# Performance work log

Measured on AMD Instinct MI355X. Metric: run time of the kernel, lower is better.

The kernel has to match this reference:

```python
import jax, jax.numpy as jnp
import numpy as np

T, B, NC, NM, H = 256, 2048, 3, 125, 256  # time, batch, classes, measures, hidden
IN = NC + NM


def setup_inputs() -> dict:
    key = jax.random.key(0)
    ks = jax.random.split(key, 12)
    seq = jax.random.normal(ks[0], (T, B, IN), jnp.float32)
    nan_mask = jax.random.uniform(ks[1], (T, B, IN)) < 0.1
    nan_mask = nan_mask.at[0].set(False)  # first step must be observed
    seq = jnp.where(nan_mask, jnp.nan, seq)
    s = 1.0 / np.sqrt(H)
    u = lambda k, shp: jax.random.uniform(k, shp, jnp.float32, -s, s)
    return {
        "pair_seq": seq,
        "W_ih": u(ks[2], (4 * H, IN)),
        "W_hh": u(ks[3], (4 * H, H)),
        "b_ih": u(ks[4], (4 * H,)),
        "b_hh": u(ks[5], (4 * H,)),
        "W_cat": u(ks[6], (NC, H)),
        "b_cat": u(ks[7], (NC,)),
        "W_val": u(ks[8], (NM, H)),
        "b_val": u(ks[9], (NM,)),
    }


def reference(pair_seq, W_ih, W_hh, b_ih, b_hh, W_cat, b_cat, W_val, b_val):
    cat_seq = pair_seq[:, :, :NC]
    val_seq = pair_seq[:, :, NC:]
    bsz = pair_seq.shape[1]
    h0 = jnp.zeros((bsz, H), pair_seq.dtype)
    c0 = jnp.zeros((bsz, H), pair_seq.dtype)
    # eval mode: dropout masks are all-ones, so they are identity multiplies

    def lstm_cell(x, h, c):
        gates = x @ W_ih.T + b_ih + h @ W_hh.T + b_hh  # [B, 4H]
        i, f, g, o = jnp.split(gates, 4, axis=-1)
        c2 = jax.nn.sigmoid(f) * c + jax.nn.sigmoid(i) * jnp.tanh(g)
        h2 = jax.nn.sigmoid(o) * jnp.tanh(c2)
        return h2, c2

    def step(carry, nxt):
        h, c, i_cat, i_val = carry
        cat_next, val_next = nxt
        x = jnp.concatenate([i_cat, i_val], axis=-1)
        h, c = lstm_cell(x, h, c)
        o_cat = jax.nn.softmax(h @ W_cat.T + b_cat, axis=-1)
        o_val = h @ W_val.T + b_val + i_val
        # impute NaNs in the next timestep with (detached) predictions
        i_cat2 = jnp.where(jnp.isnan(cat_next), jax.lax.stop_gradient(o_cat), cat_next)
        i_val2 = jnp.where(jnp.isnan(val_next), jax.lax.stop_gradient(o_val), val_next)
        return (h, c, i_cat2, i_val2), (o_cat, o_val)

    init = (h0, c0, cat_seq[0], val_seq[0])
    _, (out_cat, out_val) = jax.lax.scan(step, init, (cat_seq[1:], val_seq[1:]))
    return jnp.concatenate([out_cat, out_val], axis=2)  # [T-1, B, NC+NM]
```

## Files before the change

### kernel.cpp

```cpp
#include <hip/hip_runtime.h>
#include <hip/hip_bf16.h>

constexpr int TSTEPS = 255;
constexpr int XROW   = 392;

typedef __attribute__((ext_vector_type(8))) short short8;
typedef __attribute__((ext_vector_type(4))) float f32x4;
typedef __attribute__((ext_vector_type(16))) float f32x16;
typedef __attribute__((ext_vector_type(4))) int i32x4;
typedef __attribute__((ext_vector_type(2))) unsigned int u32x2;

__device__ __forceinline__ unsigned short f2bf(float f) {
    __hip_bfloat16 h = __float2bfloat16(f);
    return *reinterpret_cast<unsigned short*>(&h);
}
__device__ __forceinline__ float bf2f(unsigned short u) {
    __hip_bfloat16 h;
    *reinterpret_cast<unsigned short*>(&h) = u;
    return __bfloat162float(h);
}
__device__ __forceinline__ float sigf(float x) {
    return __builtin_amdgcn_rcpf(1.f + __expf(-x));
}
__device__ __forceinline__ float tanh_fast(float x) {
    x = fminf(fmaxf(x, -15.f), 15.f);
    float e = __expf(-2.f * x);
    return (1.f - e) * __builtin_amdgcn_rcpf(1.f + e);
}

__device__ __forceinline__ i32x4 load_coh16(const void* p) {
    i32x4 r;
    asm volatile("global_load_dwordx4 %0, %1, off sc0 sc1" : "=v"(r) : "v"(p) : "memory");
    return r;
}
__device__ __forceinline__ void store_coh16(void* p, i32x4 v) {
    asm volatile("global_store_dwordx4 %0, %1, off sc0 sc1" :: "v"(p), "v"(v) : "memory");
}

__device__ __forceinline__ void groupbar(unsigned int* cnt, unsigned int tgt, int tid) {
    asm volatile("s_waitcnt vmcnt(0)" ::: "memory");
    __syncthreads();
    if (tid == 0) {
        __hip_atomic_fetch_add(cnt, 1u, __ATOMIC_RELAXED, __HIP_MEMORY_SCOPE_AGENT);
        while (__hip_atomic_load(cnt, __ATOMIC_RELAXED, __HIP_MEMORY_SCOPE_AGENT) < tgt)
            __builtin_amdgcn_s_sleep(1);
    }
    __syncthreads();
}

__global__ void prep_kernel(const float* __restrict__ Wih, const float* __restrict__ Whh,
                            const float* __restrict__ bih, const float* __restrict__ bhh,
                            const float* __restrict__ Wcat, const float* __restrict__ bcat,
                            const float* __restrict__ Wval, const float* __restrict__ bval,
                            unsigned short* __restrict__ Wg, unsigned short* __restrict__ Wo,
                            float* __restrict__ bg, float* __restrict__ bo,
                            unsigned int* __restrict__ flags) {
    int idx = blockIdx.x * 256 + threadIdx.x;
    if (idx < 393216) {
        int j   = idx & 7;
        int l   = (idx >> 3) & 63;
        int t24 = idx >> 9;
        int kt  = t24 % 24;
        int u   = t24 / 24;
        int gm = u & 3, ss = u >> 2;
        int pm = l & 31;
        int n  = (pm & 3) * 256 + ss * 32 + gm * 8 + (pm >> 2);
        int k  = kt * 16 + (l >> 5) * 8 + j;
        float v = (k < 128) ? Wih[n * 128 + k] : Whh[n * 256 + (k - 128)];
        Wg[idx] = f2bf(v);
    } else if (idx < 425984) {
        int i2 = idx - 393216;
        int j = i2 & 7, ll = (i2 >> 3) & 63, kt = (i2 >> 9) & 15, om = i2 >> 13;
        int n = om * 32 + (ll & 31);
        int k = kt * 16 + (ll >> 5) * 8 + j;
        float v = (n < 3) ? Wcat[n * 256 + k] : Wval[(n - 3) * 256 + k];
        Wo[i2] = f2bf(v);
    } else if (idx < 427008) {
        int i3 = idx - 425984;
        bg[i3] = bih[i3] + bhh[i3];
    } else if (idx < 427136) {
        int i4 = idx - 427008;
        bo[i4] = (i4 < 3) ? bcat[i4] : bval[i4 - 3];
    } else if (idx < 428160) {
        flags[idx - 427136] = 0u;
    }
}

__global__ __launch_bounds__(512, 2) void rnn_kernel(
    const float* __restrict__ seq,
    const unsigned short* __restrict__ Wg, const unsigned short* __restrict__ Wo,
    const float* __restrict__ bg, const float* __restrict__ bo,
    unsigned short* __restrict__ hb, unsigned int* __restrict__ flags,
    float* __restrict__ out) {

    __shared__ __align__(16) unsigned short xh[64][XROW];
    __shared__ __align__(16) float bgl[128];
    __shared__ __align__(16) float obl[128];
    extern __shared__ char lds_pad[];
    (void)lds_pad;

    const int tid = threadIdx.x;
    const int wv  = tid >> 6, l = tid & 63;
    const int c   = l & 31, lh = l >> 5;
    const int s   = blockIdx.x >> 5;
    const int r   = blockIdx.x & 31;
    const int row0 = r * 64;
    const int hm  = wv >> 1;
    const int bn  = wv & 1;
    const int R   = bn * 32 + c;
    const bool hm0lh0 = (hm == 0) && (lh == 0);

    unsigned int* cnt = flags + r * 16;

    short8 wga[24], woa[16];
    {
        const short8* WgV = reinterpret_cast<const short8*>(Wg);
        const short8* WoV = reinterpret_cast<const short8*>(Wo);
#pragma unroll
        for (int kt = 0; kt < 24; ++kt) wga[kt] = WgV[(size_t)(((s * 4 + hm) * 24 + kt) * 64) + l];
#pragma unroll
        for (int kt = 0; kt < 16; ++kt) woa[kt] = WoV[(size_t)((hm * 16 + kt) * 64) + l];
    }

    if (tid < 128) {
        int gm_ = tid >> 5, lh_ = (tid >> 4) & 1, i_ = tid & 15;
        int pm = (i_ & 3) + 8 * (i_ >> 2) + 4 * lh_;
        bgl[tid] = bg[(pm & 3) * 256 + s * 32 + gm_ * 8 + (pm >> 2)];
        obl[tid] = bo[gm_ * 32 + 8 * (i_ >> 2) + 4 * lh_ + (i_ & 3)];
    }

#pragma unroll
    for (int i = 0; i < 4; ++i) {
        int ch = i * 512 + tid;
        int row = ch >> 5, c4 = ch & 31;
        f32x4 v = *reinterpret_cast<const f32x4*>(seq + (size_t)(row0 + row) * 128 + c4 * 4);
        unsigned short* p = &xh[row][c4 * 4];
        p[0] = f2bf(v[0]); p[1] = f2bf(v[1]); p[2] = f2bf(v[2]); p[3] = f2bf(v[3]);
    }
    {
        short8 z = {0, 0, 0, 0, 0, 0, 0, 0};
#pragma unroll
        for (int i = 0; i < 4; ++i) {
            int ch = i * 512 + tid;
            int row = ch >> 5, k8 = ch & 31;
            *reinterpret_cast<short8*>(&xh[row][128 + k8 * 8]) = z;
        }
    }

    unsigned int xv[8];
    {
        const float* sp0 = seq + (size_t)(row0 + R) * 128 + hm * 32 + 4 * lh;
#pragma unroll
        for (int g = 0; g < 4; ++g) {
            f32x4 v = *reinterpret_cast<const f32x4*>(sp0 + 8 * g);
            xv[2 * g]     = (unsigned int)f2bf(v[0]) | ((unsigned int)f2bf(v[1]) << 16);
            xv[2 * g + 1] = (unsigned int)f2bf(v[2]) | ((unsigned int)f2bf(v[3]) << 16);
        }
    }

    float cst[4] = {0.f, 0.f, 0.f, 0.f};
    const float* bgp = &bgl[(hm * 2 + lh) * 16];
    const float* obp = &obl[(hm * 2 + lh) * 16];
    const unsigned short* xrow = &xh[R][0];

    __syncthreads();

    for (int t = 0; t < TSTEPS; ++t) {
        f32x4 sq[4];
        if (t < TSTEPS - 1) {
            const float* sp = seq + ((size_t)(t + 1) * 2048 + row0 + R) * 128 + hm * 32 + 4 * lh;
#pragma unroll
            for (int g = 0; g < 4; ++g) sq[g] = *reinterpret_cast<const f32x4*>(sp + 8 * g);
        }

        f32x16 acc, accB;
#pragma unroll
        for (int i = 0; i < 16; ++i) { acc[i] = bgp[i]; accB[i] = 0.f; }
        __builtin_amdgcn_s_setprio(1);
#pragma unroll
        for (int kt = 0; kt < 24; kt += 2) {
            short8 b0 = *reinterpret_cast<const short8*>(xrow + kt * 16 + lh * 8);
            short8 b1 = *reinterpret_cast<const short8*>(xrow + (kt + 1) * 16 + lh * 8);
            acc  = __builtin_amdgcn_mfma_f32_32x32x16_bf16(wga[kt], b0, acc, 0, 0, 0);
            accB = __builtin_amdgcn_mfma_f32_32x32x16_bf16(wga[kt + 1], b1, accB, 0, 0, 0);
        }
        __builtin_amdgcn_s_setprio(0);
#pragma unroll
        for (int i = 0; i < 16; ++i) acc[i] += accB[i];

        float hn[4];
#pragma unroll
        for (int g = 0; g < 4; ++g) {
            float cn = sigf(acc[4 * g + 1]) * cst[g] + sigf(acc[4 * g]) * tanh_fast(acc[4 * g + 2]);
            hn[g] = sigf(acc[4 * g + 3]) * tanh_fast(cn);
            cst[g] = cn;
        }
        {
            i32x4 hw;
#pragma unroll
            for (int g = 0; g < 4; ++g) {
                float other = __shfl_xor(hn[g], 32);
                unsigned short lo = f2bf(lh ? other : hn[g]);
                unsigned short hi = f2bf(lh ? hn[g] : other);
                hw[g] = (int)((unsigned int)lo | ((unsigned int)hi << 16));
            }
            if (lh == 0) {
                char* hp = (char*)hb + (size_t)(t & 1) * 1048576 + (size_t)r * 32768
                         + (size_t)R * 512 + s * 64 + hm * 16;
                store_coh16(hp, hw);
            }
        }

        groupbar(cnt, 8u * (t + 1), tid);

        {
            const unsigned short* hsrc = hb + (size_t)(t & 1) * 524288 + (size_t)r * 16384;
            i32x4 hv[4];
#pragma unroll
            for (int i = 0; i < 4; ++i) {
                int ch = i * 512 + tid;
                hv[i] = load_coh16(hsrc + (size_t)((ch >> 5) * 256 + (ch & 31) * 8));
            }
            asm volatile("s_waitcnt vmcnt(0)" ::: "memory");
            __builtin_amdgcn_sched_barrier(0);
#pragma unroll
            for (int i = 0; i < 4; ++i) {
                int ch = i * 512 + tid;
                *reinterpret_cast<i32x4*>(&xh[ch >> 5][128 + (ch & 31) * 8]) = hv[i];
            }
        }
        __syncthreads();

        f32x16 acc2, acc2B;
#pragma unroll
        for (int i = 0; i < 16; ++i) { acc2[i] = obp[i]; acc2B[i] = 0.f; }
        __builtin_amdgcn_s_setprio(1);
#pragma unroll
        for (int kt = 0; kt < 16; kt += 2) {
            short8 b0 = *reinterpret_cast<const short8*>(xrow + 128 + kt * 16 + lh * 8);
            short8 b1 = *reinterpret_cast<const short8*>(xrow + 128 + (kt + 1) * 16 + lh * 8);
            acc2  = __builtin_amdgcn_mfma_f32_32x32x16_bf16(woa[kt], b0, acc2, 0, 0, 0);
            acc2B = __builtin_amdgcn_mfma_f32_32x32x16_bf16(woa[kt + 1], b1, acc2B, 0, 0, 0);
        }
        __builtin_amdgcn_s_setprio(0);

        float vv[16];
#pragma unroll
        for (int g = 0; g < 4; ++g) {
#pragma unroll
            for (int j = 0; j < 4; ++j) {
                int i = 4 * g + j;
                float v = acc2[i] + acc2B[i];
                unsigned short x16 = (unsigned short)(xv[2 * g + (j >> 1)] >> ((j & 1) * 16));
                bool isCat = (g == 0) && (j < 3) && hm0lh0;
                if (!isCat) v += bf2f(x16);
                vv[i] = v;
            }
        }
        if (hm0lh0) {
            float mx = fmaxf(fmaxf(vv[0], vv[1]), vv[2]);
            float e0 = __expf(vv[0] - mx), e1 = __expf(vv[1] - mx), e2 = __expf(vv[2] - mx);
            float rs = __builtin_amdgcn_rcpf(e0 + e1 + e2);
            vv[0] = e0 * rs; vv[1] = e1 * rs; vv[2] = e2 * rs;
        }

        if (hm == (s >> 1)) {
            int gp = (s & 1) * 2;
            size_t ob0 = ((size_t)t * 2048 + row0 + R) * 128 + hm * 32 + 4 * lh;
            f32x4 o0 = {vv[4 * gp], vv[4 * gp + 1], vv[4 * gp + 2], vv[4 * gp + 3]};
            f32x4 o1 = {vv[4 * gp + 4], vv[4 * gp + 5], vv[4 * gp + 6], vv[4 * gp + 7]};
            *reinterpret_cast<f32x4*>(out + ob0 + 8 * gp) = o0;
            *reinterpret_cast<f32x4*>(out + ob0 + 8 * gp + 8) = o1;
        }
        if (t < TSTEPS - 1) {
#pragma unroll
            for (int g = 0; g < 4; ++g) {
                unsigned int w0 = 0, w1 = 0;
#pragma unroll
                for (int j = 0; j < 4; ++j) {
                    unsigned short s16 = f2bf(sq[g][j]);
                    bool nan = (s16 & 0x7fff) > 0x7f80;
                    unsigned short nv = nan ? f2bf(vv[4 * g + j]) : s16;
                    if (j < 2) w0 |= (unsigned int)nv << (16 * j);
                    else       w1 |= (unsigned int)nv << (16 * (j - 2));
                }
                xv[2 * g] = w0; xv[2 * g + 1] = w1;
                u32x2 wp = {w0, w1};
                *reinterpret_cast<u32x2*>(&xh[R][hm * 32 + 8 * g + 4 * lh]) = wp;
            }
        }
        __syncthreads();
    }
}

extern "C" void kernel_launch(void* const* d_in, const int* in_sizes, int n_in,
                              void* d_out, int out_size, void* d_ws, size_t ws_size,
                              hipStream_t stream) {
    const float* seq  = (const float*)d_in[0];
    const float* Wih  = (const float*)d_in[1];
    const float* Whh  = (const float*)d_in[2];
    const float* bih  = (const float*)d_in[3];
    const float* bhh  = (const float*)d_in[4];
    const float* Wcat = (const float*)d_in[5];
    const float* bcat = (const float*)d_in[6];
    const float* Wval = (const float*)d_in[7];
    const float* bval = (const float*)d_in[8];

    char* ws = (char*)d_ws;
    unsigned short* Wg    = (unsigned short*)(ws);
    unsigned short* Wo    = (unsigned short*)(ws + 786432);
    float*          bgp   = (float*)(ws + 851968);
    float*          bop   = (float*)(ws + 856064);
    unsigned int*   flags = (unsigned int*)(ws + 856576);
    unsigned short* hbuf  = (unsigned short*)(ws + 860672);

    prep_kernel<<<1673, 256, 0, stream>>>(Wih, Whh, bih, bhh, Wcat, bcat, Wval, bval,
                                          Wg, Wo, bgp, bop, flags);
    rnn_kernel<<<256, 512, 32768, stream>>>(seq, Wg, Wo, bgp, bop, hbuf, flags, (float*)d_out);
}
```

Baseline: 1.145 ms.

## Load hidden state directly into MFMA operand registers, skip LDS round-trip

The hidden-state exchange buffer is re-laid out so each lane can global-load its MFMA B-operand fragments directly into registers. The output projection then runs on those registers without the LDS staging and the __syncthreads that preceded it. Only two waves write the loaded h into LDS for the next step's gate GEMM, and these writes are interleaved with the MFMAs. The load is split into two halves with a partial waitcnt so compute can start early. It also drops the dual-accumulator split, packs the next-step inputs to bf16 early, and reads the current inputs back from LDS instead of holding them in registers. This trades more global load traffic per wave and register pressure for fewer barriers on the critical serial path.

Result: slower. 1.697 ms (+48.3%).

```diff
diff --git a/kernel.cpp b/kernel.cpp
--- a/kernel.cpp
+++ b/kernel.cpp
@@ -28,8 +28,8 @@
     return (1.f - e) * __builtin_amdgcn_rcpf(1.f + e);
 }
 
-__device__ __forceinline__ i32x4 load_coh16(const void* p) {
-    i32x4 r;
+__device__ __forceinline__ short8 load_coh16s(const void* p) {
+    short8 r;
     asm volatile("global_load_dwordx4 %0, %1, off sc0 sc1" : "=v"(r) : "v"(p) : "memory");
     return r;
 }
@@ -142,19 +142,7 @@
 #pragma unroll
         for (int i = 0; i < 4; ++i) {
             int ch = i * 512 + tid;
-            int row = ch >> 5, k8 = ch & 31;
-            *reinterpret_cast<short8*>(&xh[row][128 + k8 * 8]) = z;
-        }
-    }
-
-    unsigned int xv[8];
-    {
-        const float* sp0 = seq + (size_t)(row0 + R) * 128 + hm * 32 + 4 * lh;
-#pragma unroll
-        for (int g = 0; g < 4; ++g) {
-            f32x4 v = *reinterpret_cast<const f32x4*>(sp0 + 8 * g);
-            xv[2 * g]     = (unsigned int)f2bf(v[0]) | ((unsigned int)f2bf(v[1]) << 16);
-            xv[2 * g + 1] = (unsigned int)f2bf(v[2]) | ((unsigned int)f2bf(v[3]) << 16);
+            *reinterpret_cast<short8*>(&xh[ch >> 5][128 + (ch & 31) * 8]) = z;
         }
     }
 
@@ -166,11 +154,15 @@
     __syncthreads();
 
     for (int t = 0; t < TSTEPS; ++t) {
-        f32x4 sq[4];
+        unsigned int sqb[8];
         if (t < TSTEPS - 1) {
             const float* sp = seq + ((size_t)(t + 1) * 2048 + row0 + R) * 128 + hm * 32 + 4 * lh;
 #pragma unroll
-            for (int g = 0; g < 4; ++g) sq[g] = *reinterpret_cast<const f32x4*>(sp + 8 * g);
+            for (int g = 0; g < 4; ++g) {
+                f32x4 v = *reinterpret_cast<const f32x4*>(sp + 8 * g);
+                sqb[2 * g]     = (unsigned)f2bf(v[0]) | ((unsigned)f2bf(v[1]) << 16);
+                sqb[2 * g + 1] = (unsigned)f2bf(v[2]) | ((unsigned)f2bf(v[3]) << 16);
+            }
         }
 
         f32x16 acc, accB;
@@ -202,56 +194,62 @@
                 float other = __shfl_xor(hn[g], 32);
                 unsigned short lo = f2bf(lh ? other : hn[g]);
                 unsigned short hi = f2bf(lh ? hn[g] : other);
-                hw[g] = (int)((unsigned int)lo | ((unsigned int)hi << 16));
+                hw[g] = (int)((unsigned)lo | ((unsigned)hi << 16));
             }
             if (lh == 0) {
                 char* hp = (char*)hb + (size_t)(t & 1) * 1048576 + (size_t)r * 32768
-                         + (size_t)R * 512 + s * 64 + hm * 16;
+                         + (size_t)(s * 4 + hm) * 1024 + (size_t)R * 16;
                 store_coh16(hp, hw);
             }
         }
 
         groupbar(cnt, 8u * (t + 1), tid);
 
-        {
-            const unsigned short* hsrc = hb + (size_t)(t & 1) * 524288 + (size_t)r * 16384;
-            i32x4 hv[4];
-#pragma unroll
-            for (int i = 0; i < 4; ++i) {
-                int ch = i * 512 + tid;
-                hv[i] = load_coh16(hsrc + (size_t)((ch >> 5) * 256 + (ch & 31) * 8));
-            }
-            asm volatile("s_waitcnt vmcnt(0)" ::: "memory");
-            __builtin_amdgcn_sched_barrier(0);
-#pragma unroll
-            for (int i = 0; i < 4; ++i) {
-                int ch = i * 512 + tid;
-                *reinterpret_cast<i32x4*>(&xh[ch >> 5][128 + (ch & 31) * 8]) = hv[i];
-            }
-        }
-        __syncthreads();
-
-        f32x16 acc2, acc2B;
-#pragma unroll
-        for (int i = 0; i < 16; ++i) { acc2[i] = obp[i]; acc2B[i] = 0.f; }
+        const char* hbase = (const char*)hb + (size_t)(t & 1) * 1048576
+                          + (size_t)r * 32768 + (size_t)lh * 1024 + (size_t)R * 16;
+        short8 hv0[8], hv1[8];
+        __builtin_amdgcn_sched_barrier(0);
+#pragma unroll
+        for (int q = 0; q < 8; ++q) hv0[q] = load_coh16s(hbase + (size_t)q * 2048);
+#pragma unroll
+        for (int q = 0; q < 8; ++q) hv1[q] = load_coh16s(hbase + (size_t)(8 + q) * 2048);
+        f32x16 acc2;
+#pragma unroll
+        for (int i = 0; i < 16; ++i) acc2[i] = obp[i];
+        asm volatile("s_waitcnt vmcnt(8)" ::: "memory");
+        __builtin_amdgcn_sched_barrier(0);
         __builtin_amdgcn_s_setprio(1);
 #pragma unroll
-        for (int kt = 0; kt < 16; kt += 2) {
-            short8 b0 = *reinterpret_cast<const short8*>(xrow + 128 + kt * 16 + lh * 8);
-            short8 b1 = *reinterpret_cast<const short8*>(xrow + 128 + (kt + 1) * 16 + lh * 8);
-            acc2  = __builtin_amdgcn_mfma_f32_32x32x16_bf16(woa[kt], b0, acc2, 0, 0, 0);
-            acc2B = __builtin_amdgcn_mfma_f32_32x32x16_bf16(woa[kt + 1], b1, acc2B, 0, 0, 0);
-        }
+        for (int kt = 0; kt < 8; ++kt)
+            acc2 = __builtin_amdgcn_mfma_f32_32x32x16_bf16(woa[kt], hv0[kt], acc2, 0, 0, 0);
         __builtin_amdgcn_s_setprio(0);
+        if (wv < 2 && t < TSTEPS - 1) {
+#pragma unroll
+            for (int q = 0; q < 8; ++q)
+                *reinterpret_cast<short8*>(&xh[R][128 + q * 16 + lh * 8]) = hv0[q];
+        }
+        asm volatile("s_waitcnt vmcnt(0)" ::: "memory");
+        __builtin_amdgcn_sched_barrier(0);
+        __builtin_amdgcn_s_setprio(1);
+#pragma unroll
+        for (int kt = 0; kt < 8; ++kt)
+            acc2 = __builtin_amdgcn_mfma_f32_32x32x16_bf16(woa[8 + kt], hv1[kt], acc2, 0, 0, 0);
+        __builtin_amdgcn_s_setprio(0);
+        if (wv < 2 && t < TSTEPS - 1) {
+#pragma unroll
+            for (int q = 0; q < 8; ++q)
+                *reinterpret_cast<short8*>(&xh[R][256 + q * 16 + lh * 8]) = hv1[q];
+        }
 
         float vv[16];
 #pragma unroll
         for (int g = 0; g < 4; ++g) {
+            u32x2 xw = *reinterpret_cast<const u32x2*>(&xh[R][hm * 32 + 8 * g + 4 * lh]);
 #pragma unroll
             for (int j = 0; j < 4; ++j) {
                 int i = 4 * g + j;
-                float v = acc2[i] + acc2B[i];
-                unsigned short x16 = (unsigned short)(xv[2 * g + (j >> 1)] >> ((j & 1) * 16));
+                float v = acc2[i];
+                unsigned short x16 = (unsigned short)(xw[j >> 1] >> ((j & 1) * 16));
                 bool isCat = (g == 0) && (j < 3) && hm0lh0;
                 if (!isCat) v += bf2f(x16);
                 vv[i] = v;
@@ -278,13 +276,12 @@
                 unsigned int w0 = 0, w1 = 0;
 #pragma unroll
                 for (int j = 0; j < 4; ++j) {
-                    unsigned short s16 = f2bf(sq[g][j]);
+                    unsigned short s16 = (unsigned short)(sqb[2 * g + (j >> 1)] >> ((j & 1) * 16));
                     bool nan = (s16 & 0x7fff) > 0x7f80;
                     unsigned short nv = nan ? f2bf(vv[4 * g + j]) : s16;
-                    if (j < 2) w0 |= (unsigned int)nv << (16 * j);
-                    else       w1 |= (unsigned int)nv << (16 * (j - 2));
+                    if (j < 2) w0 |= (unsigned)nv << (16 * j);
+                    else       w1 |= (unsigned)nv << (16 * (j - 2));
                 }
-                xv[2 * g] = w0; xv[2 * g + 1] = w1;
                 u32x2 wp = {w0, w1};
                 *reinterpret_cast<u32x2*>(&xh[R][hm * 32 + 8 * g + 4 * lh]) = wp;
             }
```
